# Optimization experiments

Hardware: AMD Instinct MI355X
Metric: run time of the kernel (lower is better)

The kernel has to match this reference:

```python
import jax, jax.numpy as jnp
import numpy as np

EMBED = 1024
HEADS = 16
NQ = 32        # n_qubits_transformer
NQF = 32       # n_qubits_ffn
DK = NQ // HEADS
EPS = 1e-5


def layernorm(x, g, b):
    mu = jnp.mean(x, axis=-1, keepdims=True)
    var = jnp.var(x, axis=-1, keepdims=True)
    return (x - mu) * jax.lax.rsqrt(var + EPS) * g + b


def setup_inputs() -> dict:
    key = jax.random.key(0)
    ks = jax.random.split(key, 6)
    B, S = 8, 1024
    return {
        "x": jax.random.normal(ks[0], (B, S, EMBED), dtype=jnp.float32),
        "theta_attn": jax.random.normal(ks[1], (NQ,), dtype=jnp.float32),
        "theta_ffn": jax.random.normal(ks[2], (NQF,), dtype=jnp.float32),
        "w_combine": jax.random.normal(ks[3], (EMBED, NQ), dtype=jnp.float32) * 0.05,
        "w_ffn1": jax.random.normal(ks[4], (4096, NQF), dtype=jnp.float32) * 0.05,
        "w_ffn2": jax.random.normal(ks[5], (EMBED, 4096), dtype=jnp.float32) * 0.02,
        "g1": jnp.ones((EMBED,), jnp.float32),
        "b1": jnp.zeros((EMBED,), jnp.float32),
        "g2": jnp.ones((EMBED,), jnp.float32),
        "b2": jnp.zeros((EMBED,), jnp.float32),
    }


def quantum_measure(x_slice, theta):
    # |0> -RX(x)-> -RY(theta)-> <Z>  ==  cos(theta) * cos(x)  per wire (no entanglement)
    return jnp.cos(theta) * jnp.cos(x_slice)


def reference(x, theta_attn, theta_ffn, w_combine, w_ffn1, w_ffn2, g1, b1, g2, b2):
    B, S, _ = x.shape
    # --- quantum multi-head attention (q = k = v from circuit measurements) ---
    qv = quantum_measure(x[..., :NQ], theta_attn)                    # [B,S,NQ]
    q = qv.reshape(B, S, HEADS, DK).transpose(0, 2, 1, 3)            # [B,H,S,dk]
    scores = jnp.einsum("bhsd,bhtd->bhst", q, q) / jnp.sqrt(jnp.float32(DK))
    probs = jax.nn.softmax(scores, axis=-1)
    attn = jnp.einsum("bhst,bhtd->bhsd", probs, q)                   # [B,H,S,dk]
    attn = attn.transpose(0, 2, 1, 3).reshape(B, S, NQ)
    attn = attn @ w_combine.T                                        # [B,S,E]
    x1 = layernorm(x + attn, g1, b1)
    # --- quantum feed-forward ---
    qf = quantum_measure(x1[..., :NQF], theta_ffn)                   # [B,S,NQF]
    h = jax.nn.relu(qf @ w_ffn1.T)                                   # [B,S,ffn]
    ffn = h @ w_ffn2.T                                               # [B,S,E]
    return layernorm(x1 + ffn, g2, b2)
```

## Files before the change

### kernel.cpp

```cpp
#include <hip/hip_runtime.h>
#include <math.h>

#define EMB   1024
#define S_LEN 1024
#define NQ    32
#define HEADS 16
#define FFN   4096
#define T_TOK 8192
#define EPS   1e-5f
#define MiB   (1024ull * 1024ull)

typedef unsigned short u16;
typedef __attribute__((ext_vector_type(8))) short short8;
typedef __attribute__((ext_vector_type(4))) float float4_t;

__device__ __forceinline__ u16 f2bf(float f) {
    unsigned u = __float_as_uint(f);
    u += 0x7FFF + ((u >> 16) & 1);
    return (u16)(u >> 16);
}
__device__ __forceinline__ void async16(u16* lds, const u16* g) {
    __builtin_amdgcn_global_load_lds(
        (const __attribute__((address_space(1))) unsigned int*)g,
        (__attribute__((address_space(3))) unsigned int*)lds, 16, 0, 0);
}

#define N_W1 (FFN * NQ)
#define N_W2 (EMB * FFN)
#define N_WC (EMB * NQ)
__global__ __launch_bounds__(256) void k_conv(
        const float* __restrict__ w1, const float* __restrict__ w2,
        const float* __restrict__ wc, u16* __restrict__ w1b,
        u16* __restrict__ w2b, u16* __restrict__ wcb) {
    int idx = blockIdx.x * 256 + threadIdx.x;
    if (idx < N_W1)               w1b[idx] = f2bf(w1[idx]);
    else if (idx < N_W1 + N_W2)   w2b[idx - N_W1] = f2bf(w2[idx - N_W1]);
    else if (idx < N_W1 + N_W2 + N_WC) wcb[idx - N_W1 - N_W2] = f2bf(wc[idx - N_W1 - N_W2]);
}

__global__ __launch_bounds__(256) void k_qv(const float* __restrict__ x,
                                            const float* __restrict__ tha,
                                            float* __restrict__ qv) {
    int idx = blockIdx.x * 256 + threadIdx.x;
    int i = idx & 31;
    int t = idx >> 5;
    int b = t >> 10, s = t & 1023;
    float cv = __cosf(tha[i]) * __cosf(x[(size_t)t * EMB + i]);
    int h = i >> 1, c = i & 1;
    qv[(((size_t)(b * HEADS + h)) * S_LEN + s) * 2 + c] = cv;
}

__global__ __launch_bounds__(256) void k_attn(const float* __restrict__ qv,
                                              u16* __restrict__ attnB) {
    __shared__ __align__(16) float2 kv[S_LEN];
    int bh  = blockIdx.x;
    int tid = threadIdx.x;
    const float2* base = (const float2*)(qv + (size_t)bh * S_LEN * 2);
    for (int i = tid; i < S_LEN; i += 256) kv[i] = base[i];
    __syncthreads();
    int s = blockIdx.y * 256 + tid;
    float2 q = kv[s];
    float qx = q.x * 0.70710678f, qy = q.y * 0.70710678f;
    float den = 0.f, nx = 0.f, ny = 0.f;
#pragma unroll 4
    for (int t = 0; t < S_LEN; ++t) {
        float2 k = kv[t];
        float d = fmaf(qy, k.y, qx * k.x);
        float e = __expf(d);
        den += e;
        nx = fmaf(e, k.x, nx);
        ny = fmaf(e, k.y, ny);
    }
    float inv = 1.f / den;
    int b = bh >> 4, h = bh & 15;
    u16* o = attnB + (size_t)(b * S_LEN + s) * NQ + 2 * h;
    o[0] = f2bf(nx * inv);
    o[1] = f2bf(ny * inv);
}

__global__ __launch_bounds__(256) void k_combine_mfma(
        const u16* __restrict__ A,
        const u16* __restrict__ B,
        const float* __restrict__ X,
        float* __restrict__ Y) {
    __shared__ __align__(16) u16 sA[128 * 32];
    __shared__ __align__(16) u16 sB[128 * 32];
    int tid = threadIdx.x, lane = tid & 63, wave = tid >> 6;
    int m0 = blockIdx.y * 128, n0 = blockIdx.x * 128;
    int wm = (wave >> 1) * 64, wn = (wave & 1) * 64;
    int srow = lane >> 2, scol = (lane & 3) * 8;
#pragma unroll
    for (int i = 0; i < 2; ++i) {
        int rb = wave * 32 + i * 16;
        async16(&sA[(size_t)rb * 32], A + (size_t)(m0 + rb + srow) * 32 + scol);
        async16(&sB[(size_t)rb * 32], B + (size_t)(n0 + rb + srow) * 32 + scol);
    }
    __syncthreads();
    short8 af[4], bfr[4];
#pragma unroll
    for (int tm = 0; tm < 4; ++tm)
        af[tm] = *(const short8*)&sA[(size_t)(wm + tm * 16 + (lane & 15)) * 32 + (lane >> 4) * 8];
#pragma unroll
    for (int tn = 0; tn < 4; ++tn)
        bfr[tn] = *(const short8*)&sB[(size_t)(wn + tn * 16 + (lane & 15)) * 32 + (lane >> 4) * 8];
    float4_t zero = {0.f, 0.f, 0.f, 0.f};
#pragma unroll
    for (int tm = 0; tm < 4; ++tm) {
        int mr = m0 + wm + tm * 16 + (lane >> 4) * 4;
#pragma unroll
        for (int tn = 0; tn < 4; ++tn) {
            float4_t acc = __builtin_amdgcn_mfma_f32_16x16x32_bf16(af[tm], bfr[tn], zero, 0, 0, 0);
            int nc = n0 + wn + tn * 16 + (lane & 15);
#pragma unroll
            for (int r = 0; r < 4; ++r) {
                size_t off = (size_t)(mr + r) * EMB + nc;
                Y[off] = acc[r] + X[off];
            }
        }
    }
}

__global__ __launch_bounds__(256) void k_ln1(float* __restrict__ x1,
                                             const float* __restrict__ g1,
                                             const float* __restrict__ b1,
                                             const float* __restrict__ thf,
                                             u16* __restrict__ qf) {
    __shared__ float red[8];
    int t = blockIdx.x;
    int tid = threadIdx.x, lane = tid & 63, wave = tid >> 6;
    int e0 = tid * 4;
    float* row = x1 + (size_t)t * EMB;
    float4 v4 = *(const float4*)(row + e0);
    float v[4] = {v4.x, v4.y, v4.z, v4.w};
    float sm = v[0] + v[1] + v[2] + v[3];
    float sq = v[0]*v[0] + v[1]*v[1] + v[2]*v[2] + v[3]*v[3];
    for (int o = 32; o > 0; o >>= 1) {
        sm += __shfl_xor(sm, o, 64);
        sq += __shfl_xor(sq, o, 64);
    }
    if (lane == 0) { red[wave * 2] = sm; red[wave * 2 + 1] = sq; }
    __syncthreads();
    sm = red[0] + red[2] + red[4] + red[6];
    sq = red[1] + red[3] + red[5] + red[7];
    float mu  = sm * (1.f / EMB);
    float var = sq * (1.f / EMB) - mu * mu;
    float rs  = rsqrtf(var + EPS);
    float4 o4;
    float* ov = (float*)&o4;
#pragma unroll
    for (int j = 0; j < 4; ++j) {
        int e = e0 + j;
        float y = (v[j] - mu) * rs * g1[e] + b1[e];
        ov[j] = y;
        if (e < NQ)
            qf[(size_t)t * NQ + e] = f2bf(__cosf(thf[e]) * __cosf(y));
    }
    *(float4*)(row + e0) = o4;
}

__global__ __launch_bounds__(256) void k_h(
        const u16* __restrict__ QF,
        const u16* __restrict__ W1,
        u16* __restrict__ H) {
    __shared__ __align__(16) u16 sA[128 * 32];
    __shared__ __align__(16) u16 sB[128 * 32];
    int tid = threadIdx.x, lane = tid & 63, wave = tid >> 6;
    int m0 = blockIdx.y * 128, n0 = blockIdx.x * 128;
    int wm = (wave >> 1) * 64, wn = (wave & 1) * 64;
    int srow = lane >> 2, scol = (lane & 3) * 8;
#pragma unroll
    for (int i = 0; i < 2; ++i) {
        int rb = wave * 32 + i * 16;
        async16(&sA[(size_t)rb * 32], QF + (size_t)(m0 + rb + srow) * 32 + scol);
        async16(&sB[(size_t)rb * 32], W1 + (size_t)(n0 + rb + srow) * 32 + scol);
    }
    __syncthreads();
    short8 af[4], bfr[4];
#pragma unroll
    for (int tm = 0; tm < 4; ++tm)
        af[tm] = *(const short8*)&sA[(size_t)(wm + tm * 16 + (lane & 15)) * 32 + (lane >> 4) * 8];
#pragma unroll
    for (int tn = 0; tn < 4; ++tn)
        bfr[tn] = *(const short8*)&sB[(size_t)(wn + tn * 16 + (lane & 15)) * 32 + (lane >> 4) * 8];
    float4_t zero = {0.f, 0.f, 0.f, 0.f};
#pragma unroll
    for (int tm = 0; tm < 4; ++tm) {
        int mr = m0 + wm + tm * 16 + (lane >> 4) * 4;
#pragma unroll
        for (int tn = 0; tn < 4; ++tn) {
            float4_t acc = __builtin_amdgcn_mfma_f32_16x16x32_bf16(af[tm], bfr[tn], zero, 0, 0, 0);
            int nc = n0 + wn + tn * 16 + (lane & 15);
#pragma unroll
            for (int r = 0; r < 4; ++r)
                H[(size_t)(mr + r) * FFN + nc] = f2bf(fmaxf(acc[r], 0.f));
        }
    }
}

__global__ __launch_bounds__(256, 2) void k_ffn2_db(
        const u16* __restrict__ H,
        const u16* __restrict__ W2,
        const float* __restrict__ X1,
        float* __restrict__ Y) {
    __shared__ __align__(16) u16 smem[32768];
    const int tid = threadIdx.x, lane = tid & 63, wave = tid >> 6;
    const int wm = wave >> 1, wn = wave & 1;

    int bid = blockIdx.x;
    int lid = (bid & 7) * 64 + (bid >> 3);
    const int m0 = (lid >> 3) * 128, n0 = (lid & 7) * 128;

    u16* A0 = smem;          u16* B0 = smem + 8192;
    u16* A1 = smem + 16384;  u16* B1 = smem + 24576;

    const int srow = tid >> 3;
    const int scol = ((tid & 7) ^ (srow & 7)) << 3;
    const int cb0 = ((0  + ((lane >> 4) * 16)) ^ ((lane & 7) << 4)) >> 1;
    const int cb1 = ((64 + ((lane >> 4) * 16)) ^ ((lane & 7) << 4)) >> 1;
    const int arow = lane & 15;

    auto stage = [&](u16* sA, u16* sB, int kt) {
#pragma unroll
        for (int j = 0; j < 4; ++j)
            async16(sA + (j * 32 + wave * 8) * 64,
                    H + (size_t)(m0 + j * 32 + srow) * FFN + kt + scol);
#pragma unroll
        for (int j = 0; j < 4; ++j)
            async16(sB + (j * 32 + wave * 8) * 64,
                    W2 + (size_t)(n0 + j * 32 + srow) * FFN + kt + scol);
    };

    float4_t acc[4][4];
    float4_t zero = {0.f, 0.f, 0.f, 0.f};
#pragma unroll
    for (int i = 0; i < 4; ++i)
#pragma unroll
        for (int j = 0; j < 4; ++j) acc[i][j] = zero;

    u16 *cA = A0, *cB = B0, *nA = A1, *nB = B1;
    stage(cA, cB, 0);

#pragma unroll 1
    for (int t = 0; t < 64; ++t) {
        if (t + 1 < 64) {
            stage(nA, nB, (t + 1) * 64);
            asm volatile("s_waitcnt vmcnt(8)" ::: "memory");
        } else {
            asm volatile("s_waitcnt vmcnt(0)" ::: "memory");
        }
        __builtin_amdgcn_s_barrier();

        short8 af0[4], af1[4], bf0[4], bf1[4];
#pragma unroll
        for (int f = 0; f < 4; ++f) {
            af0[f] = *(const short8*)(cA + (wm * 64 + f * 16 + arow) * 64 + cb0);
            af1[f] = *(const short8*)(cA + (wm * 64 + f * 16 + arow) * 64 + cb1);
        }
#pragma unroll
        for (int f = 0; f < 4; ++f) {
            bf0[f] = *(const short8*)(cB + (wn * 64 + f * 16 + arow) * 64 + cb0);
            bf1[f] = *(const short8*)(cB + (wn * 64 + f * 16 + arow) * 64 + cb1);
        }
        __builtin_amdgcn_s_setprio(1);
#pragma unroll
        for (int i = 0; i < 4; ++i)
#pragma unroll
            for (int j = 0; j < 4; ++j)
                acc[i][j] = __builtin_amdgcn_mfma_f32_16x16x32_bf16(af0[i], bf0[j], acc[i][j], 0, 0, 0);
#pragma unroll
        for (int i = 0; i < 4; ++i)
#pragma unroll
            for (int j = 0; j < 4; ++j)
                acc[i][j] = __builtin_amdgcn_mfma_f32_16x16x32_bf16(af1[i], bf1[j], acc[i][j], 0, 0, 0);
        __builtin_amdgcn_s_setprio(0);
        __builtin_amdgcn_s_barrier();

        u16* tA = cA; cA = nA; nA = tA;
        u16* tB = cB; cB = nB; nB = tB;
    }

#pragma unroll
    for (int i = 0; i < 4; ++i) {
        int mr = m0 + wm * 64 + i * 16 + (lane >> 4) * 4;
#pragma unroll
        for (int j = 0; j < 4; ++j) {
            int nc = n0 + wn * 64 + j * 16 + (lane & 15);
#pragma unroll
            for (int r = 0; r < 4; ++r) {
                size_t off = (size_t)(mr + r) * EMB + nc;
                Y[off] = acc[i][j][r] + X1[off];
            }
        }
    }
}

__global__ __launch_bounds__(256) void k_ffn_fused(
        const u16* __restrict__ QF,
        const u16* __restrict__ W1,
        const u16* __restrict__ W2,
        const float* __restrict__ X1,
        float* __restrict__ Y) {
    const int K = FFN, N = EMB;
    __shared__ __align__(16) u16 sW[64 * 32];
    __shared__ __align__(16) u16 sA[128 * 64];
    __shared__ __align__(16) u16 sB[128 * 64];
    int tid = threadIdx.x, lane = tid & 63, wave = tid >> 6;
    int m0 = blockIdx.y * 128, n0 = blockIdx.x * 128;
    int wm = (wave >> 1) * 64, wn = (wave & 1) * 64;

    short8 aq[2];
#pragma unroll
    for (int tm2 = 0; tm2 < 2; ++tm2) {
        int m = m0 + wave * 32 + tm2 * 16 + (lane & 15);
        aq[tm2] = *(const short8*)(QF + (size_t)m * 32 + (lane >> 4) * 8);
    }
    const u16* gB = W2 + (size_t)(n0 + wave * 32 + (lane >> 3)) * K + (lane & 7) * 8;
    const u16* gW = W1 + (size_t)(wave * 16 + (lane >> 2)) * 32 + (lane & 3) * 8;

    float4_t acc[4][4];
    float4_t zero = {0.f, 0.f, 0.f, 0.f};
#pragma unroll
    for (int tm = 0; tm < 4; ++tm)
#pragma unroll
        for (int tn = 0; tn < 4; ++tn) acc[tm][tn] = zero;

    for (int kt = 0; kt < K; kt += 64) {
        async16(&sW[(size_t)(wave * 16) * 32], gW + (size_t)kt * 32);
#pragma unroll
        for (int i = 0; i < 4; ++i)
            async16(&sB[(size_t)(wave * 32 + i * 8) * 64], gB + (size_t)i * 8 * K + kt);
        __syncthreads();

        int r0 = (lane >> 4) * 4;
#pragma unroll
        for (int tm2 = 0; tm2 < 2; ++tm2) {
            int mrow = wave * 32 + tm2 * 16;
#pragma unroll
            for (int tf = 0; tf < 4; ++tf) {
                short8 bw = *(const short8*)&sW[(size_t)(tf * 16 + (lane & 15)) * 32 + (lane >> 4) * 8];
                float4_t d = __builtin_amdgcn_mfma_f32_16x16x32_bf16(aq[tm2], bw, zero, 0, 0, 0);
                int cc = tf * 16 + (lane & 15);
#pragma unroll
                for (int r = 0; r < 4; ++r)
                    sA[(size_t)(mrow + r0 + r) * 64 + cc] = f2bf(fmaxf(d[r], 0.f));
            }
        }
        __syncthreads();

#pragma unroll
        for (int kk = 0; kk < 2; ++kk) {
            short8 af[4], bfr[4];
#pragma unroll
            for (int tm = 0; tm < 4; ++tm)
                af[tm] = *(const short8*)&sA[(size_t)(wm + tm * 16 + (lane & 15)) * 64 + kk * 32 + (lane >> 4) * 8];
#pragma unroll
            for (int tn = 0; tn < 4; ++tn)
                bfr[tn] = *(const short8*)&sB[(size_t)(wn + tn * 16 + (lane & 15)) * 64 + kk * 32 + (lane >> 4) * 8];
#pragma unroll
            for (int tm = 0; tm < 4; ++tm)
#pragma unroll
                for (int tn = 0; tn < 4; ++tn)
                    acc[tm][tn] = __builtin_amdgcn_mfma_f32_16x16x32_bf16(af[tm], bfr[tn], acc[tm][tn], 0, 0, 0);
        }
        __syncthreads();
    }
#pragma unroll
    for (int tm = 0; tm < 4; ++tm) {
        int mr = m0 + wm + tm * 16 + (lane >> 4) * 4;
#pragma unroll
        for (int tn = 0; tn < 4; ++tn) {
            int nc = n0 + wn + tn * 16 + (lane & 15);
#pragma unroll
            for (int r = 0; r < 4; ++r) {
                size_t off = (size_t)(mr + r) * N + nc;
                Y[off] = acc[tm][tn][r] + X1[off];
            }
        }
    }
}

__global__ __launch_bounds__(256) void k_ln2(float* __restrict__ y,
                                             const float* __restrict__ g2,
                                             const float* __restrict__ b2) {
    __shared__ float red[8];
    int t = blockIdx.x;
    int tid = threadIdx.x, lane = tid & 63, wave = tid >> 6;
    int e0 = tid * 4;
    float* row = y + (size_t)t * EMB;
    float4 v4 = *(const float4*)(row + e0);
    float v[4] = {v4.x, v4.y, v4.z, v4.w};
    float sm = v[0] + v[1] + v[2] + v[3];
    float sq = v[0]*v[0] + v[1]*v[1] + v[2]*v[2] + v[3]*v[3];
    for (int o = 32; o > 0; o >>= 1) {
        sm += __shfl_xor(sm, o, 64);
        sq += __shfl_xor(sq, o, 64);
    }
    if (lane == 0) { red[wave * 2] = sm; red[wave * 2 + 1] = sq; }
    __syncthreads();
    sm = red[0] + red[2] + red[4] + red[6];
    sq = red[1] + red[3] + red[5] + red[7];
    float mu  = sm * (1.f / EMB);
    float var = sq * (1.f / EMB) - mu * mu;
    float rs  = rsqrtf(var + EPS);
    float4 o4;
    o4.x = (v[0] - mu) * rs * g2[e0 + 0] + b2[e0 + 0];
    o4.y = (v[1] - mu) * rs * g2[e0 + 1] + b2[e0 + 1];
    o4.z = (v[2] - mu) * rs * g2[e0 + 2] + b2[e0 + 2];
    o4.w = (v[3] - mu) * rs * g2[e0 + 3] + b2[e0 + 3];
    *(float4*)(row + e0) = o4;
}

extern "C" void kernel_launch(void* const* d_in, const int* in_sizes, int n_in,
                              void* d_out, int out_size, void* d_ws, size_t ws_size,
                              hipStream_t stream) {
    const float* x   = (const float*)d_in[0];
    const float* tha = (const float*)d_in[1];
    const float* thf = (const float*)d_in[2];
    const float* wc  = (const float*)d_in[3];
    const float* w1  = (const float*)d_in[4];
    const float* w2  = (const float*)d_in[5];
    const float* g1  = (const float*)d_in[6];
    const float* b1  = (const float*)d_in[7];
    const float* g2  = (const float*)d_in[8];
    const float* b2  = (const float*)d_in[9];
    float* out = (float*)d_out;

    char* ws = (char*)d_ws;
    float* x1    = (float*)(ws);
    float* qv    = (float*)(ws + 32 * MiB);
    u16*   attnB = (u16*)  (ws + 33 * MiB);
    u16*   qf    = (u16*)  (ws + 34 * MiB);
    u16*   w1b   = (u16*)  (ws + 35 * MiB);
    u16*   w2b   = (u16*)  (ws + 36 * MiB);
    u16*   wcb   = (u16*)  (ws + 44 * MiB);
    u16*   hbuf  = (u16*)  (ws + 48 * MiB);

    const bool split = ws_size >= (size_t)112 * MiB;

    k_conv<<<(N_W1 + N_W2 + N_WC + 255) / 256, 256, 0, stream>>>(
        w1, w2, wc, w1b, w2b, wcb);
    k_qv<<<T_TOK * NQ / 256, 256, 0, stream>>>(x, tha, qv);
    k_attn<<<dim3(128, 4), 256, 0, stream>>>(qv, attnB);
    k_combine_mfma<<<dim3(EMB / 128, T_TOK / 128), 256, 0, stream>>>(
        attnB, wcb, x, x1);
    k_ln1<<<T_TOK, 256, 0, stream>>>(x1, g1, b1, thf, qf);
    if (split) {
        k_h<<<dim3(FFN / 128, T_TOK / 128), 256, 0, stream>>>(qf, w1b, hbuf);
        k_ffn2_db<<<dim3(512), 256, 0, stream>>>(hbuf, w2b, x1, out);
    } else {
        k_ffn_fused<<<dim3(EMB / 128, T_TOK / 128), 256, 0, stream>>>(
            qf, w1b, w2b, x1, out);
    }
    k_ln2<<<T_TOK, 256, 0, stream>>>(out, g2, b2);
}
```

Measured before the change: 285.0 us.

## Load FFN2 A operand directly into registers and merge qv prep into weight conversion

The FFN2 GEMM no longer stages the H (A) tile through LDS. Each wave loads its A fragments straight from global memory into registers, double-buffered across two K steps, while only W2 stays in LDS. This halves LDS use and removes the LDS round trip for A, at the cost of more registers and less coalesced A loads duplicated across the wn waves. Separately, the qv cosine kernel is folded into the weight-conversion launch to save one kernel launch.

```diff
diff --git a/kernel.cpp b/kernel.cpp
--- a/kernel.cpp
+++ b/kernel.cpp
@@ -28,26 +28,24 @@
 #define N_W1 (FFN * NQ)
 #define N_W2 (EMB * FFN)
 #define N_WC (EMB * NQ)
-__global__ __launch_bounds__(256) void k_conv(
+__global__ __launch_bounds__(256) void k_prep(
         const float* __restrict__ w1, const float* __restrict__ w2,
-        const float* __restrict__ wc, u16* __restrict__ w1b,
-        u16* __restrict__ w2b, u16* __restrict__ wcb) {
+        const float* __restrict__ wc, const float* __restrict__ x,
+        const float* __restrict__ tha,
+        u16* __restrict__ w1b, u16* __restrict__ w2b, u16* __restrict__ wcb,
+        float* __restrict__ qv) {
     int idx = blockIdx.x * 256 + threadIdx.x;
+    if (idx < T_TOK * NQ) {
+        int i = idx & 31;
+        int t = idx >> 5;
+        int b = t >> 10, s = t & 1023;
+        float cv = __cosf(tha[i]) * __cosf(x[(size_t)t * EMB + i]);
+        int h = i >> 1, c = i & 1;
+        qv[(((size_t)(b * HEADS + h)) * S_LEN + s) * 2 + c] = cv;
+    }
     if (idx < N_W1)               w1b[idx] = f2bf(w1[idx]);
     else if (idx < N_W1 + N_W2)   w2b[idx - N_W1] = f2bf(w2[idx - N_W1]);
     else if (idx < N_W1 + N_W2 + N_WC) wcb[idx - N_W1 - N_W2] = f2bf(wc[idx - N_W1 - N_W2]);
-}
-
-__global__ __launch_bounds__(256) void k_qv(const float* __restrict__ x,
-                                            const float* __restrict__ tha,
-                                            float* __restrict__ qv) {
-    int idx = blockIdx.x * 256 + threadIdx.x;
-    int i = idx & 31;
-    int t = idx >> 5;
-    int b = t >> 10, s = t & 1023;
-    float cv = __cosf(tha[i]) * __cosf(x[(size_t)t * EMB + i]);
-    int h = i >> 1, c = i & 1;
-    qv[(((size_t)(b * HEADS + h)) * S_LEN + s) * 2 + c] = cv;
 }
 
 __global__ __launch_bounds__(256) void k_attn(const float* __restrict__ qv,
@@ -197,12 +195,12 @@
     }
 }
 
-__global__ __launch_bounds__(256, 2) void k_ffn2_db(
+__global__ __launch_bounds__(256, 2) void k_ffn2_ar(
         const u16* __restrict__ H,
         const u16* __restrict__ W2,
         const float* __restrict__ X1,
         float* __restrict__ Y) {
-    __shared__ __align__(16) u16 smem[32768];
+    __shared__ __align__(16) u16 smem[16384];
     const int tid = threadIdx.x, lane = tid & 63, wave = tid >> 6;
     const int wm = wave >> 1, wn = wave & 1;
 
@@ -210,8 +208,8 @@
     int lid = (bid & 7) * 64 + (bid >> 3);
     const int m0 = (lid >> 3) * 128, n0 = (lid & 7) * 128;
 
-    u16* A0 = smem;          u16* B0 = smem + 8192;
-    u16* A1 = smem + 16384;  u16* B1 = smem + 24576;
+    u16* B0 = smem;
+    u16* B1 = smem + 8192;
 
     const int srow = tid >> 3;
     const int scol = ((tid & 7) ^ (srow & 7)) << 3;
@@ -219,16 +217,22 @@
     const int cb1 = ((64 + ((lane >> 4) * 16)) ^ ((lane & 7) << 4)) >> 1;
     const int arow = lane & 15;
 
-    auto stage = [&](u16* sA, u16* sB, int kt) {
-#pragma unroll
-        for (int j = 0; j < 4; ++j)
-            async16(sA + (j * 32 + wave * 8) * 64,
-                    H + (size_t)(m0 + j * 32 + srow) * FFN + kt + scol);
+    const u16* Hb = H + (size_t)(m0 + wm * 64 + arow) * FFN + (lane >> 4) * 8;
+
+    auto stageB = [&](u16* sB, int kt) {
 #pragma unroll
         for (int j = 0; j < 4; ++j)
             async16(sB + (j * 32 + wave * 8) * 64,
                     W2 + (size_t)(n0 + j * 32 + srow) * FFN + kt + scol);
     };
+    auto loadA = [&](short8 (&dst)[8], int kt) {
+#pragma unroll
+        for (int kk = 0; kk < 2; ++kk)
+#pragma unroll
+            for (int f = 0; f < 4; ++f)
+                dst[kk * 4 + f] =
+                    *(const short8*)(Hb + (size_t)(f * 16) * FFN + kt + kk * 32);
+    };
 
     float4_t acc[4][4];
     float4_t zero = {0.f, 0.f, 0.f, 0.f};
@@ -237,46 +241,62 @@
 #pragma unroll
         for (int j = 0; j < 4; ++j) acc[i][j] = zero;
 
-    u16 *cA = A0, *cB = B0, *nA = A1, *nB = B1;
-    stage(cA, cB, 0);
+    short8 afA[8], afB[8];
+    stageB(B0, 0);   loadA(afA, 0);
+    stageB(B1, 64);  loadA(afB, 64);
 
 #pragma unroll 1
-    for (int t = 0; t < 64; ++t) {
-        if (t + 1 < 64) {
-            stage(nA, nB, (t + 1) * 64);
-            asm volatile("s_waitcnt vmcnt(8)" ::: "memory");
-        } else {
-            asm volatile("s_waitcnt vmcnt(0)" ::: "memory");
-        }
+    for (int t = 0; t < 64; t += 2) {
+        asm volatile("s_waitcnt vmcnt(12)" ::: "memory");
         __builtin_amdgcn_s_barrier();
-
-        short8 af0[4], af1[4], bf0[4], bf1[4];
-#pragma unroll
-        for (int f = 0; f < 4; ++f) {
-            af0[f] = *(const short8*)(cA + (wm * 64 + f * 16 + arow) * 64 + cb0);
-            af1[f] = *(const short8*)(cA + (wm * 64 + f * 16 + arow) * 64 + cb1);
-        }
-#pragma unroll
-        for (int f = 0; f < 4; ++f) {
-            bf0[f] = *(const short8*)(cB + (wn * 64 + f * 16 + arow) * 64 + cb0);
-            bf1[f] = *(const short8*)(cB + (wn * 64 + f * 16 + arow) * 64 + cb1);
-        }
-        __builtin_amdgcn_s_setprio(1);
-#pragma unroll
-        for (int i = 0; i < 4; ++i)
-#pragma unroll
-            for (int j = 0; j < 4; ++j)
-                acc[i][j] = __builtin_amdgcn_mfma_f32_16x16x32_bf16(af0[i], bf0[j], acc[i][j], 0, 0, 0);
-#pragma unroll
-        for (int i = 0; i < 4; ++i)
-#pragma unroll
-            for (int j = 0; j < 4; ++j)
-                acc[i][j] = __builtin_amdgcn_mfma_f32_16x16x32_bf16(af1[i], bf1[j], acc[i][j], 0, 0, 0);
-        __builtin_amdgcn_s_setprio(0);
+        {
+            short8 bf0[4], bf1[4];
+#pragma unroll
+            for (int f = 0; f < 4; ++f) {
+                bf0[f] = *(const short8*)(B0 + (wn * 64 + f * 16 + arow) * 64 + cb0);
+                bf1[f] = *(const short8*)(B0 + (wn * 64 + f * 16 + arow) * 64 + cb1);
+            }
+            __builtin_amdgcn_s_setprio(1);
+#pragma unroll
+            for (int i = 0; i < 4; ++i)
+#pragma unroll
+                for (int j = 0; j < 4; ++j)
+                    acc[i][j] = __builtin_amdgcn_mfma_f32_16x16x32_bf16(afA[i], bf0[j], acc[i][j], 0, 0, 0);
+#pragma unroll
+            for (int i = 0; i < 4; ++i)
+#pragma unroll
+                for (int j = 0; j < 4; ++j)
+                    acc[i][j] = __builtin_amdgcn_mfma_f32_16x16x32_bf16(afA[4 + i], bf1[j], acc[i][j], 0, 0, 0);
+            __builtin_amdgcn_s_setprio(0);
+        }
         __builtin_amdgcn_s_barrier();
-
-        u16* tA = cA; cA = nA; nA = tA;
-        u16* tB = cB; cB = nB; nB = tB;
+        if (t + 2 < 64) { stageB(B0, (t + 2) * 64); loadA(afA, (t + 2) * 64); }
+
+        if (t + 2 < 64) asm volatile("s_waitcnt vmcnt(12)" ::: "memory");
+        else            asm volatile("s_waitcnt vmcnt(0)"  ::: "memory");
+        __builtin_amdgcn_s_barrier();
+        {
+            short8 bf0[4], bf1[4];
+#pragma unroll
+            for (int f = 0; f < 4; ++f) {
+                bf0[f] = *(const short8*)(B1 + (wn * 64 + f * 16 + arow) * 64 + cb0);
+                bf1[f] = *(const short8*)(B1 + (wn * 64 + f * 16 + arow) * 64 + cb1);
+            }
+            __builtin_amdgcn_s_setprio(1);
+#pragma unroll
+            for (int i = 0; i < 4; ++i)
+#pragma unroll
+                for (int j = 0; j < 4; ++j)
+                    acc[i][j] = __builtin_amdgcn_mfma_f32_16x16x32_bf16(afB[i], bf0[j], acc[i][j], 0, 0, 0);
+#pragma unroll
+            for (int i = 0; i < 4; ++i)
+#pragma unroll
+                for (int j = 0; j < 4; ++j)
+                    acc[i][j] = __builtin_amdgcn_mfma_f32_16x16x32_bf16(afB[4 + i], bf1[j], acc[i][j], 0, 0, 0);
+            __builtin_amdgcn_s_setprio(0);
+        }
+        __builtin_amdgcn_s_barrier();
+        if (t + 3 < 64) { stageB(B1, (t + 3) * 64); loadA(afB, (t + 3) * 64); }
     }
 
 #pragma unroll
@@ -437,16 +457,15 @@
 
     const bool split = ws_size >= (size_t)112 * MiB;
 
-    k_conv<<<(N_W1 + N_W2 + N_WC + 255) / 256, 256, 0, stream>>>(
-        w1, w2, wc, w1b, w2b, wcb);
-    k_qv<<<T_TOK * NQ / 256, 256, 0, stream>>>(x, tha, qv);
+    k_prep<<<(N_W1 + N_W2 + N_WC + 255) / 256, 256, 0, stream>>>(
+        w1, w2, wc, x, tha, w1b, w2b, wcb, qv);
     k_attn<<<dim3(128, 4), 256, 0, stream>>>(qv, attnB);
     k_combine_mfma<<<dim3(EMB / 128, T_TOK / 128), 256, 0, stream>>>(
         attnB, wcb, x, x1);
     k_ln1<<<T_TOK, 256, 0, stream>>>(x1, g1, b1, thf, qf);
     if (split) {
         k_h<<<dim3(FFN / 128, T_TOK / 128), 256, 0, stream>>>(qf, w1b, hbuf);
-        k_ffn2_db<<<dim3(512), 256, 0, stream>>>(hbuf, w2b, x1, out);
+        k_ffn2_ar<<<dim3(512), 256, 0, stream>>>(hbuf, w2b, x1, out);
     } else {
         k_ffn_fused<<<dim3(EMB / 128, T_TOK / 128), 256, 0, stream>>>(
             qf, w1b, w2b, x1, out);
```

Result: slower. 366.5 us (+28.6%).

## Fuse combine GEMM with LayerNorm1 and merge qv into weight-conversion kernel

Applied to the files above, without the earlier changes.

The combine projection and the first LayerNorm now run in one kernel. Each block owns 16 full token rows, computes all 1024 output columns with MFMA in registers, adds the residual, reduces the row statistics across waves, and writes normalized x1 plus the cos features for the FFN. This removes one full write and re-read of the 32 MiB x1 intermediate and one launch. The qv measurement kernel is also folded into the weight-conversion launch to save a second launch. In exchange each thread holds 16 accumulator vectors, so register pressure rises, and the B fragments are read straight from global memory instead of through LDS.

```diff
diff --git a/kernel.cpp b/kernel.cpp
--- a/kernel.cpp
+++ b/kernel.cpp
@@ -28,26 +28,24 @@
 #define N_W1 (FFN * NQ)
 #define N_W2 (EMB * FFN)
 #define N_WC (EMB * NQ)
-__global__ __launch_bounds__(256) void k_conv(
+__global__ __launch_bounds__(256) void k_prep(
         const float* __restrict__ w1, const float* __restrict__ w2,
-        const float* __restrict__ wc, u16* __restrict__ w1b,
-        u16* __restrict__ w2b, u16* __restrict__ wcb) {
+        const float* __restrict__ wc, const float* __restrict__ x,
+        const float* __restrict__ tha,
+        u16* __restrict__ w1b, u16* __restrict__ w2b, u16* __restrict__ wcb,
+        float* __restrict__ qv) {
     int idx = blockIdx.x * 256 + threadIdx.x;
+    if (idx < T_TOK * NQ) {
+        int i = idx & 31;
+        int t = idx >> 5;
+        int b = t >> 10, s = t & 1023;
+        float cv = __cosf(tha[i]) * __cosf(x[(size_t)t * EMB + i]);
+        int h = i >> 1, c = i & 1;
+        qv[(((size_t)(b * HEADS + h)) * S_LEN + s) * 2 + c] = cv;
+    }
     if (idx < N_W1)               w1b[idx] = f2bf(w1[idx]);
     else if (idx < N_W1 + N_W2)   w2b[idx - N_W1] = f2bf(w2[idx - N_W1]);
     else if (idx < N_W1 + N_W2 + N_WC) wcb[idx - N_W1 - N_W2] = f2bf(wc[idx - N_W1 - N_W2]);
-}
-
-__global__ __launch_bounds__(256) void k_qv(const float* __restrict__ x,
-                                            const float* __restrict__ tha,
-                                            float* __restrict__ qv) {
-    int idx = blockIdx.x * 256 + threadIdx.x;
-    int i = idx & 31;
-    int t = idx >> 5;
-    int b = t >> 10, s = t & 1023;
-    float cv = __cosf(tha[i]) * __cosf(x[(size_t)t * EMB + i]);
-    int h = i >> 1, c = i & 1;
-    qv[(((size_t)(b * HEADS + h)) * S_LEN + s) * 2 + c] = cv;
 }
 
 __global__ __launch_bounds__(256) void k_attn(const float* __restrict__ qv,
@@ -78,84 +76,78 @@
     o[1] = f2bf(ny * inv);
 }
 
-__global__ __launch_bounds__(256) void k_combine_mfma(
+__global__ __launch_bounds__(256) void k_combine_ln(
         const u16* __restrict__ A,
         const u16* __restrict__ B,
         const float* __restrict__ X,
-        float* __restrict__ Y) {
-    __shared__ __align__(16) u16 sA[128 * 32];
-    __shared__ __align__(16) u16 sB[128 * 32];
+        const float* __restrict__ g1, const float* __restrict__ b1,
+        const float* __restrict__ thf,
+        float* __restrict__ x1,
+        u16* __restrict__ qf) {
+    __shared__ float red[4][16][2];
     int tid = threadIdx.x, lane = tid & 63, wave = tid >> 6;
-    int m0 = blockIdx.y * 128, n0 = blockIdx.x * 128;
-    int wm = (wave >> 1) * 64, wn = (wave & 1) * 64;
-    int srow = lane >> 2, scol = (lane & 3) * 8;
-#pragma unroll
-    for (int i = 0; i < 2; ++i) {
-        int rb = wave * 32 + i * 16;
-        async16(&sA[(size_t)rb * 32], A + (size_t)(m0 + rb + srow) * 32 + scol);
-        async16(&sB[(size_t)rb * 32], B + (size_t)(n0 + rb + srow) * 32 + scol);
+    int t0 = blockIdx.x * 16;
+    int colbase = wave * 256;
+    int rrow = (lane >> 4) * 4;
+    short8 afr = *(const short8*)(A + (size_t)(t0 + (lane & 15)) * 32 + (lane >> 4) * 8);
+    float4_t acc[16];
+    float4_t zero = {0.f, 0.f, 0.f, 0.f};
+#pragma unroll
+    for (int tn = 0; tn < 16; ++tn) {
+        short8 bfr = *(const short8*)(B + (size_t)(colbase + tn * 16 + (lane & 15)) * 32 + (lane >> 4) * 8);
+        acc[tn] = __builtin_amdgcn_mfma_f32_16x16x32_bf16(afr, bfr, zero, 0, 0, 0);
+    }
+    float sm[4] = {0.f, 0.f, 0.f, 0.f}, sq[4] = {0.f, 0.f, 0.f, 0.f};
+#pragma unroll
+    for (int tn = 0; tn < 16; ++tn) {
+        int nc = colbase + tn * 16 + (lane & 15);
+#pragma unroll
+        for (int r = 0; r < 4; ++r) {
+            float v = acc[tn][r] + X[(size_t)(t0 + rrow + r) * EMB + nc];
+            acc[tn][r] = v;
+            sm[r] += v;
+            sq[r] = fmaf(v, v, sq[r]);
+        }
+    }
+#pragma unroll
+    for (int o = 1; o < 16; o <<= 1) {
+#pragma unroll
+        for (int r = 0; r < 4; ++r) {
+            sm[r] += __shfl_xor(sm[r], o, 64);
+            sq[r] += __shfl_xor(sq[r], o, 64);
+        }
+    }
+    if ((lane & 15) == 0) {
+#pragma unroll
+        for (int r = 0; r < 4; ++r) {
+            red[wave][rrow + r][0] = sm[r];
+            red[wave][rrow + r][1] = sq[r];
+        }
     }
     __syncthreads();
-    short8 af[4], bfr[4];
-#pragma unroll
-    for (int tm = 0; tm < 4; ++tm)
-        af[tm] = *(const short8*)&sA[(size_t)(wm + tm * 16 + (lane & 15)) * 32 + (lane >> 4) * 8];
-#pragma unroll
-    for (int tn = 0; tn < 4; ++tn)
-        bfr[tn] = *(const short8*)&sB[(size_t)(wn + tn * 16 + (lane & 15)) * 32 + (lane >> 4) * 8];
-    float4_t zero = {0.f, 0.f, 0.f, 0.f};
-#pragma unroll
-    for (int tm = 0; tm < 4; ++tm) {
-        int mr = m0 + wm + tm * 16 + (lane >> 4) * 4;
-#pragma unroll
-        for (int tn = 0; tn < 4; ++tn) {
-            float4_t acc = __builtin_amdgcn_mfma_f32_16x16x32_bf16(af[tm], bfr[tn], zero, 0, 0, 0);
-            int nc = n0 + wn + tn * 16 + (lane & 15);
-#pragma unroll
-            for (int r = 0; r < 4; ++r) {
-                size_t off = (size_t)(mr + r) * EMB + nc;
-                Y[off] = acc[r] + X[off];
-            }
-        }
-    }
-}
-
-__global__ __launch_bounds__(256) void k_ln1(float* __restrict__ x1,
-                                             const float* __restrict__ g1,
-                                             const float* __restrict__ b1,
-                                             const float* __restrict__ thf,
-                                             u16* __restrict__ qf) {
-    __shared__ float red[8];
-    int t = blockIdx.x;
-    int tid = threadIdx.x, lane = tid & 63, wave = tid >> 6;
-    int e0 = tid * 4;
-    float* row = x1 + (size_t)t * EMB;
-    float4 v4 = *(const float4*)(row + e0);
-    float v[4] = {v4.x, v4.y, v4.z, v4.w};
-    float sm = v[0] + v[1] + v[2] + v[3];
-    float sq = v[0]*v[0] + v[1]*v[1] + v[2]*v[2] + v[3]*v[3];
-    for (int o = 32; o > 0; o >>= 1) {
-        sm += __shfl_xor(sm, o, 64);
-        sq += __shfl_xor(sq, o, 64);
-    }
-    if (lane == 0) { red[wave * 2] = sm; red[wave * 2 + 1] = sq; }
-    __syncthreads();
-    sm = red[0] + red[2] + red[4] + red[6];
-    sq = red[1] + red[3] + red[5] + red[7];
-    float mu  = sm * (1.f / EMB);
-    float var = sq * (1.f / EMB) - mu * mu;
-    float rs  = rsqrtf(var + EPS);
-    float4 o4;
-    float* ov = (float*)&o4;
-#pragma unroll
-    for (int j = 0; j < 4; ++j) {
-        int e = e0 + j;
-        float y = (v[j] - mu) * rs * g1[e] + b1[e];
-        ov[j] = y;
-        if (e < NQ)
-            qf[(size_t)t * NQ + e] = f2bf(__cosf(thf[e]) * __cosf(y));
-    }
-    *(float4*)(row + e0) = o4;
+    float mu[4], rs[4];
+#pragma unroll
+    for (int r = 0; r < 4; ++r) {
+        float s = red[0][rrow + r][0] + red[1][rrow + r][0] +
+                  red[2][rrow + r][0] + red[3][rrow + r][0];
+        float q = red[0][rrow + r][1] + red[1][rrow + r][1] +
+                  red[2][rrow + r][1] + red[3][rrow + r][1];
+        float m = s * (1.f / EMB);
+        mu[r] = m;
+        rs[r] = rsqrtf(q * (1.f / EMB) - m * m + EPS);
+    }
+#pragma unroll
+    for (int tn = 0; tn < 16; ++tn) {
+        int nc = colbase + tn * 16 + (lane & 15);
+        float g = g1[nc], bb = b1[nc];
+#pragma unroll
+        for (int r = 0; r < 4; ++r) {
+            float y = (acc[tn][r] - mu[r]) * rs[r] * g + bb;
+            x1[(size_t)(t0 + rrow + r) * EMB + nc] = y;
+            if (nc < NQ)
+                qf[(size_t)(t0 + rrow + r) * NQ + nc] = f2bf(__cosf(thf[nc]) * __cosf(y));
+        }
+    }
 }
 
 __global__ __launch_bounds__(256) void k_h(
@@ -437,13 +429,11 @@
 
     const bool split = ws_size >= (size_t)112 * MiB;
 
-    k_conv<<<(N_W1 + N_W2 + N_WC + 255) / 256, 256, 0, stream>>>(
-        w1, w2, wc, w1b, w2b, wcb);
-    k_qv<<<T_TOK * NQ / 256, 256, 0, stream>>>(x, tha, qv);
+    k_prep<<<(N_W1 + N_W2 + N_WC + 255) / 256, 256, 0, stream>>>(
+        w1, w2, wc, x, tha, w1b, w2b, wcb, qv);
     k_attn<<<dim3(128, 4), 256, 0, stream>>>(qv, attnB);
-    k_combine_mfma<<<dim3(EMB / 128, T_TOK / 128), 256, 0, stream>>>(
-        attnB, wcb, x, x1);
-    k_ln1<<<T_TOK, 256, 0, stream>>>(x1, g1, b1, thf, qf);
+    k_combine_ln<<<T_TOK / 16, 256, 0, stream>>>(
+        attnB, wcb, x, g1, b1, thf, x1, qf);
     if (split) {
         k_h<<<dim3(FFN / 128, T_TOK / 128), 256, 0, stream>>>(qf, w1b, hbuf);
         k_ffn2_db<<<dim3(512), 256, 0, stream>>>(hbuf, w2b, x1, out);
```

Result: faster. 251.3 us (-11.8%).
